# Performance work log

Measured on AMD Instinct MI355X. Metric: run time of the kernel, lower is better.

Reference implementation:

```python
import jax, jax.numpy as jnp
import numpy as np

B, D, H = 65536, 64, 512  # batch, input_dim (even), hidden_dim; num_layers=4 -> 4 Linears


def setup_inputs() -> dict:
    key = jax.random.key(0)
    ks = jax.random.split(key, 10)
    s_in = 1.0 / np.sqrt(D)
    s_h = 1.0 / np.sqrt(H)
    return {
        "t": jnp.zeros((1,), jnp.float32),
        "x": jax.random.normal(ks[0], (B, D), jnp.float32),
        "W0": jax.random.uniform(ks[1], (D, H), jnp.float32, -s_in, s_in),
        "b0": jax.random.uniform(ks[2], (H,), jnp.float32, -s_in, s_in),
        "W1": jax.random.uniform(ks[3], (H, H), jnp.float32, -s_h, s_h),
        "b1": jax.random.uniform(ks[4], (H,), jnp.float32, -s_h, s_h),
        "W2": jax.random.uniform(ks[5], (H, H), jnp.float32, -s_h, s_h),
        "b2": jax.random.uniform(ks[6], (H,), jnp.float32, -s_h, s_h),
        "W3": jax.random.uniform(ks[7], (H, 1), jnp.float32, -s_h, s_h),
        "b3": jax.random.uniform(ks[8], (1,), jnp.float32, -s_h, s_h),
    }


def reference(t, x, W0, b0, W1, b1, W2, b2, W3, b3):
    # Hamiltonian MLP: Linear->Tanh x3, final Linear to scalar energy per sample.
    def hamiltonian_sum(xx):
        h = jnp.tanh(xx @ W0 + b0)
        h = jnp.tanh(h @ W1 + b1)
        h = jnp.tanh(h @ W2 + b2)
        return jnp.sum(h @ W3 + b3)

    gradH = jax.grad(hamiltonian_sum)(x)  # [B, D]
    n = D // 2
    # gradH @ J.T with symplectic J == concat(gradH_p, -gradH_q)
    return jnp.concatenate([gradH[:, n:], -gradH[:, :n]], axis=1)
```

## Files before the change

### kernel.cpp

```cpp
#include <hip/hip_runtime.h>
#include <hip/hip_bf16.h>

typedef unsigned short u16;
typedef short s16x8 __attribute__((ext_vector_type(8)));
typedef float f32x4 __attribute__((ext_vector_type(4)));

#define MFMA_BF16(a, b, c) __builtin_amdgcn_mfma_f32_16x16x32_bf16((a), (b), (c), 0, 0, 0)

static constexpr int D_IN   = 64;
static constexpr int H_DIM  = 512;
static constexpr int M_TILE = 64;
static constexpr int AST    = 520;
static constexpr int XST    = 72;

__device__ __forceinline__ u16 f2bf(float f) {
  unsigned u = __builtin_bit_cast(unsigned, f);
  u += 0x7fffu + ((u >> 16) & 1u);
  return (u16)(u >> 16);
}
__device__ __forceinline__ float bfb2f(unsigned bits16) {
  return __builtin_bit_cast(float, bits16 << 16);
}
__device__ __forceinline__ float fast_tanh(float x) {
  float e = __expf(2.0f * x);
  return 1.0f - 2.0f * __builtin_amdgcn_rcpf(e + 1.0f);
}

__global__ __launch_bounds__(256) void prep_weights(const float* __restrict__ W0,
                                                    const float* __restrict__ W1,
                                                    const float* __restrict__ W2,
                                                    u16* __restrict__ ws) {
  u16* p0f = ws;
  u16* p0b = p0f + D_IN * H_DIM;
  u16* p1f = p0b + D_IN * H_DIM;
  u16* p1b = p1f + H_DIM * H_DIM;
  u16* p2f = p1b + H_DIM * H_DIM;
  u16* p2b = p2f + H_DIM * H_DIM;

  __shared__ __align__(16) u16 tile[64 * 72];

  int b = blockIdx.x;
  const float* src;
  u16 *dstf, *dstb;
  int rb, cb;
  bool isW0;
  if (b < 64) {
    src = W1; dstf = p1f; dstb = p1b; rb = b >> 3; cb = b & 7; isW0 = false;
  } else if (b < 128) {
    src = W2; dstf = p2f; dstb = p2b; rb = (b - 64) >> 3; cb = (b - 64) & 7; isW0 = false;
  } else {
    src = W0; dstf = p0f; dstb = p0b; rb = 0; cb = b - 128; isW0 = true;
  }

  const int tid = threadIdx.x;

  {
    int r = tid >> 2, cc = (tid & 3) * 16;
    const float4* s4 = (const float4*)(src + (size_t)(rb * 64 + r) * 512 + cb * 64 + cc);
    unsigned pk[8];
    #pragma unroll
    for (int v = 0; v < 4; ++v) {
      float4 f = s4[v];
      pk[v * 2]     = (unsigned)f2bf(f.x) | ((unsigned)f2bf(f.y) << 16);
      pk[v * 2 + 1] = (unsigned)f2bf(f.z) | ((unsigned)f2bf(f.w) << 16);
    }
    uint4* d = (uint4*)(tile + r * 72 + cc);
    d[0] = make_uint4(pk[0], pk[1], pk[2], pk[3]);
    d[1] = make_uint4(pk[4], pk[5], pk[6], pk[7]);
  }
  __syncthreads();

  const int c   = tid >> 6;
  const int kcl = (tid >> 5) & 1;
  const int ls  = (tid * 2) & 63;
  const int q   = ls >> 4;
  const int ln  = ls & 15;

  {
    __align__(16) u16 o[16];
    #pragma unroll
    for (int half = 0; half < 2; ++half)
      #pragma unroll
      for (int j = 0; j < 8; ++j)
        o[half * 8 + j] = tile[(kcl * 32 + q * 8 + j) * 72 + c * 16 + ln + half];
    int ntg   = 4 * cb + c;
    int kc    = 2 * rb + kcl;
    int chunk = isW0 ? (ntg * 2 + kc) : (ntg * 16 + kc);
    u16* dp = dstf + ((size_t)chunk * 64 + ls) * 8;
    *(uint4*)dp       = *(const uint4*)o;
    *(uint4*)(dp + 8) = *(const uint4*)(o + 8);
  }

  {
    const u16* rp = tile + (c * 16 + ln) * 72 + kcl * 32 + q * 8;
    s16x8 r0 = *(const s16x8*)rp;
    s16x8 r1 = *(const s16x8*)(rp + 72);
    int ntg = 4 * rb + c;
    int kc  = 2 * cb + kcl;
    u16* dp = dstb + ((size_t)(ntg * 16 + kc) * 64 + ls) * 8;
    *(s16x8*)dp       = r0;
    *(s16x8*)(dp + 8) = r1;
  }
}

#define LOAD_B4(BP, KC, BR)                                                     \
  {                                                                             \
    const u16* _sr = (BP) + ((size_t)wave << 15) + ((KC) << 9) + lane * 8;      \
    _Pragma("unroll")                                                           \
    for (int s = 0; s < 4; ++s)                                                 \
      (BR)[s] = *(const s16x8*)(_sr + (s << 13));                               \
  }

#define GEMM512_REG(BP)                                                         \
  {                                                                             \
    _Pragma("unroll") for (int mt = 0; mt < 4; ++mt)                            \
      _Pragma("unroll") for (int nt = 0; nt < 4; ++nt)                          \
        acc[mt][nt] = (f32x4){0.f, 0.f, 0.f, 0.f};                              \
    for (int kc2 = 0; kc2 < 8; ++kc2) {                                         \
      const int e = kc2 * 2;                                                    \
      {                                                                         \
        s16x8 a[4];                                                             \
        _Pragma("unroll")                                                       \
        for (int mt = 0; mt < 4; ++mt)                                          \
          a[mt] = *(const s16x8*)(buf + (mt * 16 + ln) * AST + e * 32 + q * 8); \
        _Pragma("unroll")                                                       \
        for (int nt = 0; nt < 4; ++nt)                                          \
          _Pragma("unroll")                                                     \
          for (int mt = 0; mt < 4; ++mt)                                        \
            acc[mt][nt] = MFMA_BF16(a[mt], bregA[nt], acc[mt][nt]);             \
        if (kc2 < 7) LOAD_B4(BP, e + 2, bregA);                                 \
      }                                                                         \
      const int o = e + 1;                                                      \
      {                                                                         \
        s16x8 a[4];                                                             \
        _Pragma("unroll")                                                       \
        for (int mt = 0; mt < 4; ++mt)                                          \
          a[mt] = *(const s16x8*)(buf + (mt * 16 + ln) * AST + o * 32 + q * 8); \
        _Pragma("unroll")                                                       \
        for (int nt = 0; nt < 4; ++nt)                                          \
          _Pragma("unroll")                                                     \
          for (int mt = 0; mt < 4; ++mt)                                        \
            acc[mt][nt] = MFMA_BF16(a[mt], bregB[nt], acc[mt][nt]);             \
        if (kc2 < 7) LOAD_B4(BP, o + 2, bregB);                                 \
      }                                                                         \
    }                                                                           \
  }

__global__ __launch_bounds__(512, 2) void hnn_fused(
    const float* __restrict__ x,
    const float* __restrict__ bias0,
    const float* __restrict__ bias1,
    const float* __restrict__ bias2,
    const float* __restrict__ W3,
    const u16* __restrict__ ws,
    float* __restrict__ out)
{
  const u16* p0f = ws;
  const u16* p0b = p0f + D_IN * H_DIM;
  const u16* p1f = p0b + D_IN * H_DIM;
  const u16* p1b = p1f + H_DIM * H_DIM;
  const u16* p2f = p1b + H_DIM * H_DIM;
  const u16* p2b = p2f + H_DIM * H_DIM;

  __shared__ __align__(16) u16 xs[M_TILE * XST];
  __shared__ __align__(16) u16 buf[M_TILE * AST];

  const int tid  = threadIdx.x;
  const int wave = tid >> 6;
  const int lane = tid & 63;
  const int ln   = lane & 15;
  const int q    = lane >> 4;
  const int nwb  = wave * 64;
  const int row0 = blockIdx.x * M_TILE;

  {
    int r = tid >> 3, c = (tid & 7) * 8;
    const float4* src = (const float4*)(x + (size_t)(row0 + r) * D_IN + c);
    float4 f0 = src[0];
    float4 f1 = src[1];
    u16* dst = xs + r * XST + c;
    dst[0] = f2bf(f0.x); dst[1] = f2bf(f0.y); dst[2] = f2bf(f0.z); dst[3] = f2bf(f0.w);
    dst[4] = f2bf(f1.x); dst[5] = f2bf(f1.y); dst[6] = f2bf(f1.z); dst[7] = f2bf(f1.w);
  }
  __syncthreads();

  f32x4 acc[4][4];
  s16x8 bregA[4], bregB[4];
  unsigned h0p[4][4][2];
  unsigned h1p[4][4][2];
  float bias[4];

  #pragma unroll
  for (int nt = 0; nt < 4; ++nt) bias[nt] = bias0[nwb + nt * 16 + ln];
  #pragma unroll
  for (int mt = 0; mt < 4; ++mt)
    #pragma unroll
    for (int nt = 0; nt < 4; ++nt) acc[mt][nt] = (f32x4){0.f, 0.f, 0.f, 0.f};
  {
    const u16* bpw0 = p0f + (wave << 12) + lane * 8;
    #pragma unroll
    for (int kc = 0; kc < 2; ++kc) {
      s16x8 a[4];
      #pragma unroll
      for (int mt = 0; mt < 4; ++mt)
        a[mt] = *(const s16x8*)(xs + (mt * 16 + ln) * XST + kc * 32 + q * 8);
      #pragma unroll
      for (int nt = 0; nt < 4; ++nt) {
        s16x8 b = *(const s16x8*)(bpw0 + (nt << 10) + (kc << 9));
        #pragma unroll
        for (int mt = 0; mt < 4; ++mt)
          acc[mt][nt] = MFMA_BF16(a[mt], b, acc[mt][nt]);
      }
    }
  }
  LOAD_B4(p1f, 0, bregA);
  LOAD_B4(p1f, 1, bregB);
  #pragma unroll
  for (int mt = 0; mt < 4; ++mt)
    #pragma unroll
    for (int nt = 0; nt < 4; ++nt) {
      int col = nwb + nt * 16 + ln;
      u16 u[4];
      #pragma unroll
      for (int r = 0; r < 4; ++r) {
        float th = fast_tanh(acc[mt][nt][r] + bias[nt]);
        u[r] = f2bf(th);
        buf[(mt * 16 + q * 4 + r) * AST + col] = u[r];
      }
      h0p[mt][nt][0] = (unsigned)u[0] | ((unsigned)u[1] << 16);
      h0p[mt][nt][1] = (unsigned)u[2] | ((unsigned)u[3] << 16);
    }
  __syncthreads();

  #pragma unroll
  for (int nt = 0; nt < 4; ++nt) bias[nt] = bias1[nwb + nt * 16 + ln];
  GEMM512_REG(p1f);
  __syncthreads();
  LOAD_B4(p2f, 0, bregA);
  LOAD_B4(p2f, 1, bregB);
  #pragma unroll
  for (int mt = 0; mt < 4; ++mt)
    #pragma unroll
    for (int nt = 0; nt < 4; ++nt) {
      int col = nwb + nt * 16 + ln;
      u16 u[4];
      #pragma unroll
      for (int r = 0; r < 4; ++r) {
        float th = fast_tanh(acc[mt][nt][r] + bias[nt]);
        u[r] = f2bf(th);
        buf[(mt * 16 + q * 4 + r) * AST + col] = u[r];
      }
      h1p[mt][nt][0] = (unsigned)u[0] | ((unsigned)u[1] << 16);
      h1p[mt][nt][1] = (unsigned)u[2] | ((unsigned)u[3] << 16);
    }
  __syncthreads();

  #pragma unroll
  for (int nt = 0; nt < 4; ++nt) bias[nt] = bias2[nwb + nt * 16 + ln];
  float w3v[4];
  #pragma unroll
  for (int nt = 0; nt < 4; ++nt) w3v[nt] = W3[nwb + nt * 16 + ln];
  GEMM512_REG(p2f);
  __syncthreads();
  LOAD_B4(p2b, 0, bregA);
  LOAD_B4(p2b, 1, bregB);
  #pragma unroll
  for (int mt = 0; mt < 4; ++mt)
    #pragma unroll
    for (int nt = 0; nt < 4; ++nt) {
      int col = nwb + nt * 16 + ln;
      #pragma unroll
      for (int r = 0; r < 4; ++r) {
        float th = fast_tanh(acc[mt][nt][r] + bias[nt]);
        float gz = w3v[nt] * (1.0f - th * th);
        buf[(mt * 16 + q * 4 + r) * AST + col] = f2bf(gz);
      }
    }
  __syncthreads();

  GEMM512_REG(p2b);
  __syncthreads();
  LOAD_B4(p1b, 0, bregA);
  LOAD_B4(p1b, 1, bregB);
  #pragma unroll
  for (int mt = 0; mt < 4; ++mt)
    #pragma unroll
    for (int nt = 0; nt < 4; ++nt) {
      int col = nwb + nt * 16 + ln;
      unsigned pa = h1p[mt][nt][0], pb = h1p[mt][nt][1];
      float hh[4] = { bfb2f(pa & 0xffffu), bfb2f(pa >> 16),
                      bfb2f(pb & 0xffffu), bfb2f(pb >> 16) };
      #pragma unroll
      for (int r = 0; r < 4; ++r) {
        float gz = acc[mt][nt][r] * (1.0f - hh[r] * hh[r]);
        buf[(mt * 16 + q * 4 + r) * AST + col] = f2bf(gz);
      }
    }
  __syncthreads();

  GEMM512_REG(p1b);
  __syncthreads();
  #pragma unroll
  for (int mt = 0; mt < 4; ++mt)
    #pragma unroll
    for (int nt = 0; nt < 4; ++nt) {
      int col = nwb + nt * 16 + ln;
      unsigned pa = h0p[mt][nt][0], pb = h0p[mt][nt][1];
      float hh[4] = { bfb2f(pa & 0xffffu), bfb2f(pa >> 16),
                      bfb2f(pb & 0xffffu), bfb2f(pb >> 16) };
      #pragma unroll
      for (int r = 0; r < 4; ++r) {
        float gz = acc[mt][nt][r] * (1.0f - hh[r] * hh[r]);
        buf[(mt * 16 + q * 4 + r) * AST + col] = f2bf(gz);
      }
    }
  __syncthreads();

  {
    f32x4 acc5[2];
    acc5[0] = (f32x4){0.f, 0.f, 0.f, 0.f};
    acc5[1] = (f32x4){0.f, 0.f, 0.f, 0.f};
    const int mt5 = wave & 3;
    const int nb5 = (wave >> 2) * 32;
    const u16* bp5 = p0b + ((wave >> 2) << 14) + lane * 8;
    #pragma unroll 2
    for (int kc = 0; kc < 16; ++kc) {
      s16x8 a = *(const s16x8*)(buf + (mt5 * 16 + ln) * AST + kc * 32 + q * 8);
      #pragma unroll
      for (int nt = 0; nt < 2; ++nt) {
        s16x8 b = *(const s16x8*)(bp5 + (nt << 13) + (kc << 9));
        acc5[nt] = MFMA_BF16(a, b, acc5[nt]);
      }
    }
    #pragma unroll
    for (int nt = 0; nt < 2; ++nt) {
      int g = nb5 + nt * 16 + ln;
      int c = (g < 32) ? g + 32 : g - 32;
      float s = (g < 32) ? -1.0f : 1.0f;
      #pragma unroll
      for (int r = 0; r < 4; ++r) {
        int grow = row0 + mt5 * 16 + q * 4 + r;
        out[(size_t)grow * 64 + c] = s * acc5[nt][r];
      }
    }
  }
}

extern "C" void kernel_launch(void* const* d_in, const int* in_sizes, int n_in,
                              void* d_out, int out_size, void* d_ws, size_t ws_size,
                              hipStream_t stream) {
  const float* x  = (const float*)d_in[1];
  const float* W0 = (const float*)d_in[2];
  const float* b0 = (const float*)d_in[3];
  const float* W1 = (const float*)d_in[4];
  const float* b1 = (const float*)d_in[5];
  const float* W2 = (const float*)d_in[6];
  const float* b2 = (const float*)d_in[7];
  const float* W3 = (const float*)d_in[8];
  u16* ws = (u16*)d_ws;
  float* out = (float*)d_out;

  prep_weights<<<136, 256, 0, stream>>>(W0, W1, W2, ws);
  hnn_fused<<<65536 / M_TILE, 512, 0, stream>>>(x, b0, b1, b2, W3, ws, out);
}
```

Baseline: 228.1 us.

## Switch hidden-layer GEMMs to 32x32x16 bf16 MFMA with matching weight layout

Replaces the 16x16x32 MFMA tiling (4x4 tiles per wave) with 32x32x16 MFMA (2x2 tiles per wave) for the forward and backward 512-wide GEMMs and the first layer. The weight prep kernel is changed to emit packed weights in the 32-wide N / 16-deep K chunk layout the larger MFMA expects, while W0's backward copy keeps the old layout. The larger instruction halves the number of A and B fragment loads from LDS and global memory per output and the count of issued MFMAs, at the cost of more complex epilogue indexing. The x staging store is also packed into one 16-byte LDS write.

```diff
diff --git a/kernel.cpp b/kernel.cpp
--- a/kernel.cpp
+++ b/kernel.cpp
@@ -4,8 +4,10 @@
 typedef unsigned short u16;
 typedef short s16x8 __attribute__((ext_vector_type(8)));
 typedef float f32x4 __attribute__((ext_vector_type(4)));
+typedef float f32x16 __attribute__((ext_vector_type(16)));
 
 #define MFMA_BF16(a, b, c) __builtin_amdgcn_mfma_f32_16x16x32_bf16((a), (b), (c), 0, 0, 0)
+#define MFMA32(a, b, c)    __builtin_amdgcn_mfma_f32_32x32x16_bf16((a), (b), (c), 0, 0, 0)
 
 static constexpr int D_IN   = 64;
 static constexpr int H_DIM  = 512;
@@ -24,6 +26,10 @@
 __device__ __forceinline__ float fast_tanh(float x) {
   float e = __expf(2.0f * x);
   return 1.0f - 2.0f * __builtin_amdgcn_rcpf(e + 1.0f);
+}
+__device__ __forceinline__ f32x16 zero16() {
+  f32x16 z = {0.f,0.f,0.f,0.f,0.f,0.f,0.f,0.f,0.f,0.f,0.f,0.f,0.f,0.f,0.f,0.f};
+  return z;
 }
 
 __global__ __launch_bounds__(256) void prep_weights(const float* __restrict__ W0,
@@ -70,78 +76,89 @@
   }
   __syncthreads();
 
-  const int c   = tid >> 6;
-  const int kcl = (tid >> 5) & 1;
-  const int ls  = (tid * 2) & 63;
-  const int q   = ls >> 4;
-  const int ln  = ls & 15;
+  const int cl    = tid >> 5;
+  const int nt32l = cl >> 2;
+  const int k16l  = cl & 3;
+  const int ls    = (tid & 31) * 2;
+  const int q5    = ls >> 5;
+  const int l31   = ls & 31;
 
   {
     __align__(16) u16 o[16];
     #pragma unroll
-    for (int half = 0; half < 2; ++half)
+    for (int p = 0; p < 2; ++p)
       #pragma unroll
       for (int j = 0; j < 8; ++j)
-        o[half * 8 + j] = tile[(kcl * 32 + q * 8 + j) * 72 + c * 16 + ln + half];
-    int ntg   = 4 * cb + c;
-    int kc    = 2 * rb + kcl;
-    int chunk = isW0 ? (ntg * 2 + kc) : (ntg * 16 + kc);
+        o[p * 8 + j] = tile[(k16l * 16 + q5 * 8 + j) * 72 + nt32l * 32 + l31 + p];
+    int K16MAX = isW0 ? 4 : 32;
+    int chunk = (2 * cb + nt32l) * K16MAX + (4 * rb + k16l);
     u16* dp = dstf + ((size_t)chunk * 64 + ls) * 8;
     *(uint4*)dp       = *(const uint4*)o;
     *(uint4*)(dp + 8) = *(const uint4*)(o + 8);
   }
 
-  {
+  if (!isW0) {
+    const u16* rp = tile + (nt32l * 32 + l31) * 72 + k16l * 16 + q5 * 8;
+    s16x8 r0 = *(const s16x8*)rp;
+    s16x8 r1 = *(const s16x8*)(rp + 72);
+    int chunk = (2 * rb + nt32l) * 32 + (4 * cb + k16l);
+    u16* dp = dstb + ((size_t)chunk * 64 + ls) * 8;
+    *(s16x8*)dp       = r0;
+    *(s16x8*)(dp + 8) = r1;
+  } else {
+    const int c   = tid >> 6;
+    const int kcl = (tid >> 5) & 1;
+    const int ls2 = (tid * 2) & 63;
+    const int q   = ls2 >> 4;
+    const int ln  = ls2 & 15;
     const u16* rp = tile + (c * 16 + ln) * 72 + kcl * 32 + q * 8;
     s16x8 r0 = *(const s16x8*)rp;
     s16x8 r1 = *(const s16x8*)(rp + 72);
-    int ntg = 4 * rb + c;
-    int kc  = 2 * cb + kcl;
-    u16* dp = dstb + ((size_t)(ntg * 16 + kc) * 64 + ls) * 8;
+    int kc = 2 * cb + kcl;
+    u16* dp = dstb + ((size_t)(c * 16 + kc) * 64 + ls2) * 8;
     *(s16x8*)dp       = r0;
     *(s16x8*)(dp + 8) = r1;
   }
 }
 
-#define LOAD_B4(BP, KC, BR)                                                     \
+#define LOAD_B2(BP, KS, BR)                                                     \
   {                                                                             \
-    const u16* _sr = (BP) + ((size_t)wave << 15) + ((KC) << 9) + lane * 8;      \
-    _Pragma("unroll")                                                           \
-    for (int s = 0; s < 4; ++s)                                                 \
-      (BR)[s] = *(const s16x8*)(_sr + (s << 13));                               \
-  }
-
-#define GEMM512_REG(BP)                                                         \
+    const u16* _sr = (BP) + ((size_t)wave << 15) + ((KS) << 9) + lane * 8;      \
+    (BR)[0] = *(const s16x8*)(_sr);                                             \
+    (BR)[1] = *(const s16x8*)(_sr + (1 << 14));                                 \
+  }
+
+#define GEMM512_32(BP)                                                          \
   {                                                                             \
-    _Pragma("unroll") for (int mt = 0; mt < 4; ++mt)                            \
-      _Pragma("unroll") for (int nt = 0; nt < 4; ++nt)                          \
-        acc[mt][nt] = (f32x4){0.f, 0.f, 0.f, 0.f};                              \
-    for (int kc2 = 0; kc2 < 8; ++kc2) {                                         \
-      const int e = kc2 * 2;                                                    \
+    _Pragma("unroll") for (int mt = 0; mt < 2; ++mt)                            \
+      _Pragma("unroll") for (int nt = 0; nt < 2; ++nt)                          \
+        acc[mt][nt] = zero16();                                                 \
+    for (int ks2 = 0; ks2 < 16; ++ks2) {                                        \
+      const int e = ks2 * 2;                                                    \
       {                                                                         \
-        s16x8 a[4];                                                             \
+        s16x8 a[2];                                                             \
         _Pragma("unroll")                                                       \
-        for (int mt = 0; mt < 4; ++mt)                                          \
-          a[mt] = *(const s16x8*)(buf + (mt * 16 + ln) * AST + e * 32 + q * 8); \
+        for (int mt = 0; mt < 2; ++mt)                                          \
+          a[mt] = *(const s16x8*)(buf + (mt * 32 + l31) * AST + e * 16 + q5 * 8); \
         _Pragma("unroll")                                                       \
-        for (int nt = 0; nt < 4; ++nt)                                          \
+        for (int nt = 0; nt < 2; ++nt)                                          \
           _Pragma("unroll")                                                     \
-          for (int mt = 0; mt < 4; ++mt)                                        \
-            acc[mt][nt] = MFMA_BF16(a[mt], bregA[nt], acc[mt][nt]);             \
-        if (kc2 < 7) LOAD_B4(BP, e + 2, bregA);                                 \
+          for (int mt = 0; mt < 2; ++mt)                                        \
+            acc[mt][nt] = MFMA32(a[mt], bregA[nt], acc[mt][nt]);                \
+        if (ks2 < 15) LOAD_B2(BP, e + 2, bregA);                                \
       }                                                                         \
       const int o = e + 1;                                                      \
       {                                                                         \
-        s16x8 a[4];                                                             \
+        s16x8 a[2];                                                             \
         _Pragma("unroll")                                                       \
-        for (int mt = 0; mt < 4; ++mt)                                          \
-          a[mt] = *(const s16x8*)(buf + (mt * 16 + ln) * AST + o * 32 + q * 8); \
+        for (int mt = 0; mt < 2; ++mt)                                          \
+          a[mt] = *(const s16x8*)(buf + (mt * 32 + l31) * AST + o * 16 + q5 * 8); \
         _Pragma("unroll")                                                       \
-        for (int nt = 0; nt < 4; ++nt)                                          \
+        for (int nt = 0; nt < 2; ++nt)                                          \
           _Pragma("unroll")                                                     \
-          for (int mt = 0; mt < 4; ++mt)                                        \
-            acc[mt][nt] = MFMA_BF16(a[mt], bregB[nt], acc[mt][nt]);             \
-        if (kc2 < 7) LOAD_B4(BP, o + 2, bregB);                                 \
+          for (int mt = 0; mt < 2; ++mt)                                        \
+            acc[mt][nt] = MFMA32(a[mt], bregB[nt], acc[mt][nt]);                \
+        if (ks2 < 15) LOAD_B2(BP, o + 2, bregB);                                \
       }                                                                         \
     }                                                                           \
   }
@@ -170,6 +187,8 @@
   const int lane = tid & 63;
   const int ln   = lane & 15;
   const int q    = lane >> 4;
+  const int l31  = lane & 31;
+  const int q5   = lane >> 5;
   const int nwb  = wave * 64;
   const int row0 = blockIdx.x * M_TILE;
 
@@ -178,141 +197,167 @@
     const float4* src = (const float4*)(x + (size_t)(row0 + r) * D_IN + c);
     float4 f0 = src[0];
     float4 f1 = src[1];
-    u16* dst = xs + r * XST + c;
-    dst[0] = f2bf(f0.x); dst[1] = f2bf(f0.y); dst[2] = f2bf(f0.z); dst[3] = f2bf(f0.w);
-    dst[4] = f2bf(f1.x); dst[5] = f2bf(f1.y); dst[6] = f2bf(f1.z); dst[7] = f2bf(f1.w);
-  }
-  __syncthreads();
-
-  f32x4 acc[4][4];
-  s16x8 bregA[4], bregB[4];
-  unsigned h0p[4][4][2];
-  unsigned h1p[4][4][2];
-  float bias[4];
+    unsigned pk0 = (unsigned)f2bf(f0.x) | ((unsigned)f2bf(f0.y) << 16);
+    unsigned pk1 = (unsigned)f2bf(f0.z) | ((unsigned)f2bf(f0.w) << 16);
+    unsigned pk2 = (unsigned)f2bf(f1.x) | ((unsigned)f2bf(f1.y) << 16);
+    unsigned pk3 = (unsigned)f2bf(f1.z) | ((unsigned)f2bf(f1.w) << 16);
+    uint4* dst = (uint4*)(xs + r * XST + c);
+    *dst = make_uint4(pk0, pk1, pk2, pk3);
+  }
+  __syncthreads();
+
+  f32x16 acc[2][2];
+  s16x8 bregA[2], bregB[2];
+  unsigned h0p[2][2][8];
+  unsigned h1p[2][2][8];
 
   #pragma unroll
-  for (int nt = 0; nt < 4; ++nt) bias[nt] = bias0[nwb + nt * 16 + ln];
+  for (int mt = 0; mt < 2; ++mt)
+    #pragma unroll
+    for (int nt = 0; nt < 2; ++nt) acc[mt][nt] = zero16();
+  {
+    const u16* bpw0 = p0f + ((size_t)wave << 12) + lane * 8;
+    #pragma unroll
+    for (int ks = 0; ks < 4; ++ks) {
+      s16x8 a[2];
+      #pragma unroll
+      for (int mt = 0; mt < 2; ++mt)
+        a[mt] = *(const s16x8*)(xs + (mt * 32 + l31) * XST + ks * 16 + q5 * 8);
+      #pragma unroll
+      for (int nt = 0; nt < 2; ++nt) {
+        s16x8 b = *(const s16x8*)(bpw0 + (nt << 11) + (ks << 9));
+        #pragma unroll
+        for (int mt = 0; mt < 2; ++mt)
+          acc[mt][nt] = MFMA32(a[mt], b, acc[mt][nt]);
+      }
+    }
+  }
+  LOAD_B2(p1f, 0, bregA);
+  LOAD_B2(p1f, 1, bregB);
+  {
+    float bv[2];
+    #pragma unroll
+    for (int nt = 0; nt < 2; ++nt) bv[nt] = bias0[nwb + nt * 32 + l31];
+    #pragma unroll
+    for (int mt = 0; mt < 2; ++mt)
+      #pragma unroll
+      for (int nt = 0; nt < 2; ++nt) {
+        int col = nwb + nt * 32 + l31;
+        u16* bp = buf + (mt * 32 + q5 * 4) * AST + col;
+        #pragma unroll
+        for (int g = 0; g < 4; ++g) {
+          u16 u[4];
+          #pragma unroll
+          for (int r = 0; r < 4; ++r) {
+            float th = fast_tanh(acc[mt][nt][g * 4 + r] + bv[nt]);
+            u[r] = f2bf(th);
+            bp[(g * 8 + r) * AST] = u[r];
+          }
+          h0p[mt][nt][g * 2]     = (unsigned)u[0] | ((unsigned)u[1] << 16);
+          h0p[mt][nt][g * 2 + 1] = (unsigned)u[2] | ((unsigned)u[3] << 16);
+        }
+      }
+  }
+  __syncthreads();
+
+  GEMM512_32(p1f);
+  __syncthreads();
+  LOAD_B2(p2f, 0, bregA);
+  LOAD_B2(p2f, 1, bregB);
+  {
+    float bv[2];
+    #pragma unroll
+    for (int nt = 0; nt < 2; ++nt) bv[nt] = bias1[nwb + nt * 32 + l31];
+    #pragma unroll
+    for (int mt = 0; mt < 2; ++mt)
+      #pragma unroll
+      for (int nt = 0; nt < 2; ++nt) {
+        int col = nwb + nt * 32 + l31;
+        u16* bp = buf + (mt * 32 + q5 * 4) * AST + col;
+        #pragma unroll
+        for (int g = 0; g < 4; ++g) {
+          u16 u[4];
+          #pragma unroll
+          for (int r = 0; r < 4; ++r) {
+            float th = fast_tanh(acc[mt][nt][g * 4 + r] + bv[nt]);
+            u[r] = f2bf(th);
+            bp[(g * 8 + r) * AST] = u[r];
+          }
+          h1p[mt][nt][g * 2]     = (unsigned)u[0] | ((unsigned)u[1] << 16);
+          h1p[mt][nt][g * 2 + 1] = (unsigned)u[2] | ((unsigned)u[3] << 16);
+        }
+      }
+  }
+  __syncthreads();
+
+  GEMM512_32(p2f);
+  __syncthreads();
+  LOAD_B2(p2b, 0, bregA);
+  LOAD_B2(p2b, 1, bregB);
+  {
+    float bv[2], w3v[2];
+    #pragma unroll
+    for (int nt = 0; nt < 2; ++nt) {
+      bv[nt]  = bias2[nwb + nt * 32 + l31];
+      w3v[nt] = W3[nwb + nt * 32 + l31];
+    }
+    #pragma unroll
+    for (int mt = 0; mt < 2; ++mt)
+      #pragma unroll
+      for (int nt = 0; nt < 2; ++nt) {
+        int col = nwb + nt * 32 + l31;
+        u16* bp = buf + (mt * 32 + q5 * 4) * AST + col;
+        #pragma unroll
+        for (int g = 0; g < 4; ++g)
+          #pragma unroll
+          for (int r = 0; r < 4; ++r) {
+            float th = fast_tanh(acc[mt][nt][g * 4 + r] + bv[nt]);
+            float gz = w3v[nt] * (1.0f - th * th);
+            bp[(g * 8 + r) * AST] = f2bf(gz);
+          }
+      }
+  }
+  __syncthreads();
+
+  GEMM512_32(p2b);
+  __syncthreads();
+  LOAD_B2(p1b, 0, bregA);
+  LOAD_B2(p1b, 1, bregB);
   #pragma unroll
-  for (int mt = 0; mt < 4; ++mt)
-    #pragma unroll
-    for (int nt = 0; nt < 4; ++nt) acc[mt][nt] = (f32x4){0.f, 0.f, 0.f, 0.f};
-  {
-    const u16* bpw0 = p0f + (wave << 12) + lane * 8;
-    #pragma unroll
-    for (int kc = 0; kc < 2; ++kc) {
-      s16x8 a[4];
-      #pragma unroll
-      for (int mt = 0; mt < 4; ++mt)
-        a[mt] = *(const s16x8*)(xs + (mt * 16 + ln) * XST + kc * 32 + q * 8);
-      #pragma unroll
-      for (int nt = 0; nt < 4; ++nt) {
-        s16x8 b = *(const s16x8*)(bpw0 + (nt << 10) + (kc << 9));
-        #pragma unroll
-        for (int mt = 0; mt < 4; ++mt)
-          acc[mt][nt] = MFMA_BF16(a[mt], b, acc[mt][nt]);
-      }
-    }
-  }
-  LOAD_B4(p1f, 0, bregA);
-  LOAD_B4(p1f, 1, bregB);
+  for (int mt = 0; mt < 2; ++mt)
+    #pragma unroll
+    for (int nt = 0; nt < 2; ++nt) {
+      int col = nwb + nt * 32 + l31;
+      u16* bp = buf + (mt * 32 + q5 * 4) * AST + col;
+      #pragma unroll
+      for (int g = 0; g < 4; ++g)
+        #pragma unroll
+        for (int r = 0; r < 4; ++r) {
+          unsigned pk = h1p[mt][nt][g * 2 + (r >> 1)];
+          float hh = bfb2f((r & 1) ? (pk >> 16) : (pk & 0xffffu));
+          float gz = acc[mt][nt][g * 4 + r] * (1.0f - hh * hh);
+          bp[(g * 8 + r) * AST] = f2bf(gz);
+        }
+    }
+  __syncthreads();
+
+  GEMM512_32(p1b);
+  __syncthreads();
   #pragma unroll
-  for (int mt = 0; mt < 4; ++mt)
-    #pragma unroll
-    for (int nt = 0; nt < 4; ++nt) {
-      int col = nwb + nt * 16 + ln;
-      u16 u[4];
-      #pragma unroll
-      for (int r = 0; r < 4; ++r) {
-        float th = fast_tanh(acc[mt][nt][r] + bias[nt]);
-        u[r] = f2bf(th);
-        buf[(mt * 16 + q * 4 + r) * AST + col] = u[r];
-      }
-      h0p[mt][nt][0] = (unsigned)u[0] | ((unsigned)u[1] << 16);
-      h0p[mt][nt][1] = (unsigned)u[2] | ((unsigned)u[3] << 16);
-    }
-  __syncthreads();
-
-  #pragma unroll
-  for (int nt = 0; nt < 4; ++nt) bias[nt] = bias1[nwb + nt * 16 + ln];
-  GEMM512_REG(p1f);
-  __syncthreads();
-  LOAD_B4(p2f, 0, bregA);
-  LOAD_B4(p2f, 1, bregB);
-  #pragma unroll
-  for (int mt = 0; mt < 4; ++mt)
-    #pragma unroll
-    for (int nt = 0; nt < 4; ++nt) {
-      int col = nwb + nt * 16 + ln;
-      u16 u[4];
-      #pragma unroll
-      for (int r = 0; r < 4; ++r) {
-        float th = fast_tanh(acc[mt][nt][r] + bias[nt]);
-        u[r] = f2bf(th);
-        buf[(mt * 16 + q * 4 + r) * AST + col] = u[r];
-      }
-      h1p[mt][nt][0] = (unsigned)u[0] | ((unsigned)u[1] << 16);
-      h1p[mt][nt][1] = (unsigned)u[2] | ((unsigned)u[3] << 16);
-    }
-  __syncthreads();
-
-  #pragma unroll
-  for (int nt = 0; nt < 4; ++nt) bias[nt] = bias2[nwb + nt * 16 + ln];
-  float w3v[4];
-  #pragma unroll
-  for (int nt = 0; nt < 4; ++nt) w3v[nt] = W3[nwb + nt * 16 + ln];
-  GEMM512_REG(p2f);
-  __syncthreads();
-  LOAD_B4(p2b, 0, bregA);
-  LOAD_B4(p2b, 1, bregB);
-  #pragma unroll
-  for (int mt = 0; mt < 4; ++mt)
-    #pragma unroll
-    for (int nt = 0; nt < 4; ++nt) {
-      int col = nwb + nt * 16 + ln;
-      #pragma unroll
-      for (int r = 0; r < 4; ++r) {
-        float th = fast_tanh(acc[mt][nt][r] + bias[nt]);
-        float gz = w3v[nt] * (1.0f - th * th);
-        buf[(mt * 16 + q * 4 + r) * AST + col] = f2bf(gz);
-      }
-    }
-  __syncthreads();
-
-  GEMM512_REG(p2b);
-  __syncthreads();
-  LOAD_B4(p1b, 0, bregA);
-  LOAD_B4(p1b, 1, bregB);
-  #pragma unroll
-  for (int mt = 0; mt < 4; ++mt)
-    #pragma unroll
-    for (int nt = 0; nt < 4; ++nt) {
-      int col = nwb + nt * 16 + ln;
-      unsigned pa = h1p[mt][nt][0], pb = h1p[mt][nt][1];
-      float hh[4] = { bfb2f(pa & 0xffffu), bfb2f(pa >> 16),
-                      bfb2f(pb & 0xffffu), bfb2f(pb >> 16) };
-      #pragma unroll
-      for (int r = 0; r < 4; ++r) {
-        float gz = acc[mt][nt][r] * (1.0f - hh[r] * hh[r]);
-        buf[(mt * 16 + q * 4 + r) * AST + col] = f2bf(gz);
-      }
-    }
-  __syncthreads();
-
-  GEMM512_REG(p1b);
-  __syncthreads();
-  #pragma unroll
-  for (int mt = 0; mt < 4; ++mt)
-    #pragma unroll
-    for (int nt = 0; nt < 4; ++nt) {
-      int col = nwb + nt * 16 + ln;
-      unsigned pa = h0p[mt][nt][0], pb = h0p[mt][nt][1];
-      float hh[4] = { bfb2f(pa & 0xffffu), bfb2f(pa >> 16),
-                      bfb2f(pb & 0xffffu), bfb2f(pb >> 16) };
-      #pragma unroll
-      for (int r = 0; r < 4; ++r) {
-        float gz = acc[mt][nt][r] * (1.0f - hh[r] * hh[r]);
-        buf[(mt * 16 + q * 4 + r) * AST + col] = f2bf(gz);
-      }
+  for (int mt = 0; mt < 2; ++mt)
+    #pragma unroll
+    for (int nt = 0; nt < 2; ++nt) {
+      int col = nwb + nt * 32 + l31;
+      u16* bp = buf + (mt * 32 + q5 * 4) * AST + col;
+      #pragma unroll
+      for (int g = 0; g < 4; ++g)
+        #pragma unroll
+        for (int r = 0; r < 4; ++r) {
+          unsigned pk = h0p[mt][nt][g * 2 + (r >> 1)];
+          float hh = bfb2f((r & 1) ? (pk >> 16) : (pk & 0xffffu));
+          float gz = acc[mt][nt][g * 4 + r] * (1.0f - hh * hh);
+          bp[(g * 8 + r) * AST] = f2bf(gz);
+        }
     }
   __syncthreads();
 
```

Result: slower. 260.0 us (+14.0%).

## Split row tile into two halves and overlap each epilogue with the other half's GEMM

Applied to the files above, without the earlier changes.

The 64-row block tile is split into two 32-row sub-tiles with separate accumulators and ping-pong LDS buffers. Each sub-tile's tanh or derivative epilogue is interleaved into the K-loop of the other sub-tile's GEMM, so VALU and LDS-store work overlaps MFMA instead of running in its own barrier-separated phase. Biases and W3 are loaded once up front. The cost is that each B-register load now serves only 32 rows, so weight traffic from L2 doubles, LDS use grows, and the extra accumulators and packed activations add register pressure that could cause spills.

```diff
diff --git a/kernel.cpp b/kernel.cpp
--- a/kernel.cpp
+++ b/kernel.cpp
@@ -111,39 +111,82 @@
       (BR)[s] = *(const s16x8*)(_sr + (s << 13));                               \
   }
 
-#define GEMM512_REG(BP)                                                         \
-  {                                                                             \
-    _Pragma("unroll") for (int mt = 0; mt < 4; ++mt)                            \
-      _Pragma("unroll") for (int nt = 0; nt < 4; ++nt)                          \
-        acc[mt][nt] = (f32x4){0.f, 0.f, 0.f, 0.f};                              \
-    for (int kc2 = 0; kc2 < 8; ++kc2) {                                         \
-      const int e = kc2 * 2;                                                    \
-      {                                                                         \
-        s16x8 a[4];                                                             \
-        _Pragma("unroll")                                                       \
-        for (int mt = 0; mt < 4; ++mt)                                          \
-          a[mt] = *(const s16x8*)(buf + (mt * 16 + ln) * AST + e * 32 + q * 8); \
-        _Pragma("unroll")                                                       \
-        for (int nt = 0; nt < 4; ++nt)                                          \
-          _Pragma("unroll")                                                     \
-          for (int mt = 0; mt < 4; ++mt)                                        \
-            acc[mt][nt] = MFMA_BF16(a[mt], bregA[nt], acc[mt][nt]);             \
-        if (kc2 < 7) LOAD_B4(BP, e + 2, bregA);                                 \
-      }                                                                         \
-      const int o = e + 1;                                                      \
-      {                                                                         \
-        s16x8 a[4];                                                             \
-        _Pragma("unroll")                                                       \
-        for (int mt = 0; mt < 4; ++mt)                                          \
-          a[mt] = *(const s16x8*)(buf + (mt * 16 + ln) * AST + o * 32 + q * 8); \
-        _Pragma("unroll")                                                       \
-        for (int nt = 0; nt < 4; ++nt)                                          \
-          _Pragma("unroll")                                                     \
-          for (int mt = 0; mt < 4; ++mt)                                        \
-            acc[mt][nt] = MFMA_BF16(a[mt], bregB[nt], acc[mt][nt]);             \
-        if (kc2 < 7) LOAD_B4(BP, o + 2, bregB);                                 \
-      }                                                                         \
-    }                                                                           \
+#define ZACC(ACC)                                                               \
+  _Pragma("unroll") for (int zm = 0; zm < 2; ++zm)                              \
+    _Pragma("unroll") for (int zn = 0; zn < 4; ++zn)                            \
+      ACC[zm][zn] = (f32x4){0.f, 0.f, 0.f, 0.f};
+
+#define EPI_H(MT, NT, ACC, HP, BV, DB)                                          \
+  {                                                                             \
+    float t0_ = fast_tanh(ACC[MT][NT][0] + BV[NT]);                             \
+    float t1_ = fast_tanh(ACC[MT][NT][1] + BV[NT]);                             \
+    float t2_ = fast_tanh(ACC[MT][NT][2] + BV[NT]);                             \
+    float t3_ = fast_tanh(ACC[MT][NT][3] + BV[NT]);                             \
+    u16 u0_ = f2bf(t0_), u1_ = f2bf(t1_), u2_ = f2bf(t2_), u3_ = f2bf(t3_);     \
+    u16* bp_ = (DB) + ((MT) * 16 + q * 4) * AST + nwb + (NT) * 16 + ln;         \
+    bp_[0] = u0_; bp_[AST] = u1_; bp_[2 * AST] = u2_; bp_[3 * AST] = u3_;       \
+    HP[MT][NT][0] = (unsigned)u0_ | ((unsigned)u1_ << 16);                      \
+    HP[MT][NT][1] = (unsigned)u2_ | ((unsigned)u3_ << 16);                      \
+  }
+#define EPI_G2(MT, NT, ACC, DB)                                                 \
+  {                                                                             \
+    u16* bp_ = (DB) + ((MT) * 16 + q * 4) * AST + nwb + (NT) * 16 + ln;         \
+    float t0_ = fast_tanh(ACC[MT][NT][0] + b2v[NT]);                            \
+    float t1_ = fast_tanh(ACC[MT][NT][1] + b2v[NT]);                            \
+    float t2_ = fast_tanh(ACC[MT][NT][2] + b2v[NT]);                            \
+    float t3_ = fast_tanh(ACC[MT][NT][3] + b2v[NT]);                            \
+    bp_[0]       = f2bf(w3v[NT] * (1.0f - t0_ * t0_));                          \
+    bp_[AST]     = f2bf(w3v[NT] * (1.0f - t1_ * t1_));                          \
+    bp_[2 * AST] = f2bf(w3v[NT] * (1.0f - t2_ * t2_));                          \
+    bp_[3 * AST] = f2bf(w3v[NT] * (1.0f - t3_ * t3_));                          \
+  }
+#define EPI_B(MT, NT, ACC, HP, DB)                                              \
+  {                                                                             \
+    unsigned pa_ = HP[MT][NT][0], pb_ = HP[MT][NT][1];                          \
+    float h0_ = bfb2f(pa_ & 0xffffu), h1_ = bfb2f(pa_ >> 16);                   \
+    float h2_ = bfb2f(pb_ & 0xffffu), h3_ = bfb2f(pb_ >> 16);                   \
+    u16* bp_ = (DB) + ((MT) * 16 + q * 4) * AST + nwb + (NT) * 16 + ln;         \
+    bp_[0]       = f2bf(ACC[MT][NT][0] * (1.0f - h0_ * h0_));                   \
+    bp_[AST]     = f2bf(ACC[MT][NT][1] * (1.0f - h1_ * h1_));                   \
+    bp_[2 * AST] = f2bf(ACC[MT][NT][2] * (1.0f - h2_ * h2_));                   \
+    bp_[3 * AST] = f2bf(ACC[MT][NT][3] * (1.0f - h3_ * h3_));                   \
+  }
+#define EPI_NONE(MT, NT) {}
+
+#define KSTEP(RB, ACC, BP, K2, EPIU)                                            \
+  {                                                                             \
+    s16x8 a0_ = *(const s16x8*)((RB) + (ln) * AST + (K2) * 64 + q * 8);         \
+    s16x8 a1_ = *(const s16x8*)((RB) + (16 + ln) * AST + (K2) * 64 + q * 8);    \
+    ACC[0][0] = MFMA_BF16(a0_, bregA[0], ACC[0][0]);                            \
+    ACC[1][0] = MFMA_BF16(a1_, bregA[0], ACC[1][0]);                            \
+    ACC[0][1] = MFMA_BF16(a0_, bregA[1], ACC[0][1]);                            \
+    ACC[1][1] = MFMA_BF16(a1_, bregA[1], ACC[1][1]);                            \
+    ACC[0][2] = MFMA_BF16(a0_, bregA[2], ACC[0][2]);                            \
+    ACC[1][2] = MFMA_BF16(a1_, bregA[2], ACC[1][2]);                            \
+    ACC[0][3] = MFMA_BF16(a0_, bregA[3], ACC[0][3]);                            \
+    ACC[1][3] = MFMA_BF16(a1_, bregA[3], ACC[1][3]);                            \
+    if ((K2) < 7) LOAD_B4(BP, (K2) * 2 + 2, bregA);                             \
+    EPIU((K2) >> 2, (K2) & 3);                                                  \
+    s16x8 a2_ = *(const s16x8*)((RB) + (ln) * AST + (K2) * 64 + 32 + q * 8);    \
+    s16x8 a3_ = *(const s16x8*)((RB) + (16 + ln) * AST + (K2) * 64 + 32 + q * 8); \
+    ACC[0][0] = MFMA_BF16(a2_, bregB[0], ACC[0][0]);                            \
+    ACC[1][0] = MFMA_BF16(a3_, bregB[0], ACC[1][0]);                            \
+    ACC[0][1] = MFMA_BF16(a2_, bregB[1], ACC[0][1]);                            \
+    ACC[1][1] = MFMA_BF16(a3_, bregB[1], ACC[1][1]);                            \
+    ACC[0][2] = MFMA_BF16(a2_, bregB[2], ACC[0][2]);                            \
+    ACC[1][2] = MFMA_BF16(a3_, bregB[2], ACC[1][2]);                            \
+    ACC[0][3] = MFMA_BF16(a2_, bregB[3], ACC[0][3]);                            \
+    ACC[1][3] = MFMA_BF16(a3_, bregB[3], ACC[1][3]);                            \
+    if ((K2) < 7) LOAD_B4(BP, (K2) * 2 + 3, bregB);                             \
+  }
+
+#define GEMMF(RB, ACC, BP, EPIU)                                                \
+  {                                                                             \
+    ZACC(ACC);                                                                  \
+    KSTEP(RB, ACC, BP, 0, EPIU); KSTEP(RB, ACC, BP, 1, EPIU);                   \
+    KSTEP(RB, ACC, BP, 2, EPIU); KSTEP(RB, ACC, BP, 3, EPIU);                   \
+    KSTEP(RB, ACC, BP, 4, EPIU); KSTEP(RB, ACC, BP, 5, EPIU);                   \
+    KSTEP(RB, ACC, BP, 6, EPIU); KSTEP(RB, ACC, BP, 7, EPIU);                   \
   }
 
 __global__ __launch_bounds__(512, 2) void hnn_fused(
@@ -163,7 +206,10 @@
   const u16* p2b = p2f + H_DIM * H_DIM;
 
   __shared__ __align__(16) u16 xs[M_TILE * XST];
-  __shared__ __align__(16) u16 buf[M_TILE * AST];
+  __shared__ __align__(16) u16 bufA0[32 * AST];
+  __shared__ __align__(16) u16 bufB0[32 * AST];
+  __shared__ __align__(16) u16 bufA1[32 * AST];
+  __shared__ __align__(16) u16 bufB1[32 * AST];
 
   const int tid  = threadIdx.x;
   const int wave = tid >> 6;
@@ -182,166 +228,148 @@
     dst[0] = f2bf(f0.x); dst[1] = f2bf(f0.y); dst[2] = f2bf(f0.z); dst[3] = f2bf(f0.w);
     dst[4] = f2bf(f1.x); dst[5] = f2bf(f1.y); dst[6] = f2bf(f1.z); dst[7] = f2bf(f1.w);
   }
-  __syncthreads();
-
-  f32x4 acc[4][4];
+
+  float b0v[4], b1v[4], b2v[4], w3v[4];
+  #pragma unroll
+  for (int nt = 0; nt < 4; ++nt) {
+    b0v[nt] = bias0[nwb + nt * 16 + ln];
+    b1v[nt] = bias1[nwb + nt * 16 + ln];
+    b2v[nt] = bias2[nwb + nt * 16 + ln];
+    w3v[nt] = W3[nwb + nt * 16 + ln];
+  }
+  __syncthreads();
+
+  f32x4 accA[2][4], accB[2][4];
   s16x8 bregA[4], bregB[4];
-  unsigned h0p[4][4][2];
-  unsigned h1p[4][4][2];
-  float bias[4];
-
-  #pragma unroll
-  for (int nt = 0; nt < 4; ++nt) bias[nt] = bias0[nwb + nt * 16 + ln];
-  #pragma unroll
-  for (int mt = 0; mt < 4; ++mt)
-    #pragma unroll
-    for (int nt = 0; nt < 4; ++nt) acc[mt][nt] = (f32x4){0.f, 0.f, 0.f, 0.f};
+  unsigned h0pA[2][4][2], h0pB[2][4][2];
+  unsigned h1pA[2][4][2], h1pB[2][4][2];
+
+  ZACC(accA);
   {
     const u16* bpw0 = p0f + (wave << 12) + lane * 8;
     #pragma unroll
     for (int kc = 0; kc < 2; ++kc) {
-      s16x8 a[4];
-      #pragma unroll
-      for (int mt = 0; mt < 4; ++mt)
-        a[mt] = *(const s16x8*)(xs + (mt * 16 + ln) * XST + kc * 32 + q * 8);
+      s16x8 a0 = *(const s16x8*)(xs + (ln) * XST + kc * 32 + q * 8);
+      s16x8 a1 = *(const s16x8*)(xs + (16 + ln) * XST + kc * 32 + q * 8);
       #pragma unroll
       for (int nt = 0; nt < 4; ++nt) {
         s16x8 b = *(const s16x8*)(bpw0 + (nt << 10) + (kc << 9));
-        #pragma unroll
-        for (int mt = 0; mt < 4; ++mt)
-          acc[mt][nt] = MFMA_BF16(a[mt], b, acc[mt][nt]);
+        accA[0][nt] = MFMA_BF16(a0, b, accA[0][nt]);
+        accA[1][nt] = MFMA_BF16(a1, b, accA[1][nt]);
       }
     }
   }
   LOAD_B4(p1f, 0, bregA);
   LOAD_B4(p1f, 1, bregB);
-  #pragma unroll
-  for (int mt = 0; mt < 4; ++mt)
-    #pragma unroll
-    for (int nt = 0; nt < 4; ++nt) {
-      int col = nwb + nt * 16 + ln;
-      u16 u[4];
+
+  ZACC(accB);
+  {
+    const u16* bpw0 = p0f + (wave << 12) + lane * 8;
+    #pragma unroll
+    for (int kc = 0; kc < 2; ++kc) {
+      s16x8 a0 = *(const s16x8*)(xs + (32 + ln) * XST + kc * 32 + q * 8);
+      s16x8 a1 = *(const s16x8*)(xs + (48 + ln) * XST + kc * 32 + q * 8);
       #pragma unroll
-      for (int r = 0; r < 4; ++r) {
-        float th = fast_tanh(acc[mt][nt][r] + bias[nt]);
-        u[r] = f2bf(th);
-        buf[(mt * 16 + q * 4 + r) * AST + col] = u[r];
+      for (int nt = 0; nt < 4; ++nt) {
+        s16x8 b = *(const s16x8*)(bpw0 + (nt << 10) + (kc << 9));
+        accB[0][nt] = MFMA_BF16(a0, b, accB[0][nt]);
+        accB[1][nt] = MFMA_BF16(a1, b, accB[1][nt]);
       }
-      h0p[mt][nt][0] = (unsigned)u[0] | ((unsigned)u[1] << 16);
-      h0p[mt][nt][1] = (unsigned)u[2] | ((unsigned)u[3] << 16);
-    }
-  __syncthreads();
-
-  #pragma unroll
-  for (int nt = 0; nt < 4; ++nt) bias[nt] = bias1[nwb + nt * 16 + ln];
-  GEMM512_REG(p1f);
-  __syncthreads();
+    }
+  }
+  EPI_H(0, 0, accA, h0pA, b0v, bufA0); EPI_H(0, 1, accA, h0pA, b0v, bufA0);
+  EPI_H(0, 2, accA, h0pA, b0v, bufA0); EPI_H(0, 3, accA, h0pA, b0v, bufA0);
+  EPI_H(1, 0, accA, h0pA, b0v, bufA0); EPI_H(1, 1, accA, h0pA, b0v, bufA0);
+  EPI_H(1, 2, accA, h0pA, b0v, bufA0); EPI_H(1, 3, accA, h0pA, b0v, bufA0);
+  __syncthreads();
+
+  #define EPI0T1(MT, NT) EPI_H(MT, NT, accB, h0pB, b0v, bufA1)
+  GEMMF(bufA0, accA, p1f, EPI0T1);
+  LOAD_B4(p1f, 0, bregA);
+  LOAD_B4(p1f, 1, bregB);
+  __syncthreads();
+
+  #define EPI1T0(MT, NT) EPI_H(MT, NT, accA, h1pA, b1v, bufB0)
+  GEMMF(bufA1, accB, p1f, EPI1T0);
   LOAD_B4(p2f, 0, bregA);
   LOAD_B4(p2f, 1, bregB);
-  #pragma unroll
-  for (int mt = 0; mt < 4; ++mt)
-    #pragma unroll
-    for (int nt = 0; nt < 4; ++nt) {
-      int col = nwb + nt * 16 + ln;
-      u16 u[4];
-      #pragma unroll
-      for (int r = 0; r < 4; ++r) {
-        float th = fast_tanh(acc[mt][nt][r] + bias[nt]);
-        u[r] = f2bf(th);
-        buf[(mt * 16 + q * 4 + r) * AST + col] = u[r];
-      }
-      h1p[mt][nt][0] = (unsigned)u[0] | ((unsigned)u[1] << 16);
-      h1p[mt][nt][1] = (unsigned)u[2] | ((unsigned)u[3] << 16);
-    }
-  __syncthreads();
-
-  #pragma unroll
-  for (int nt = 0; nt < 4; ++nt) bias[nt] = bias2[nwb + nt * 16 + ln];
-  float w3v[4];
-  #pragma unroll
-  for (int nt = 0; nt < 4; ++nt) w3v[nt] = W3[nwb + nt * 16 + ln];
-  GEMM512_REG(p2f);
-  __syncthreads();
+  __syncthreads();
+
+  #define EPI1T1(MT, NT) EPI_H(MT, NT, accB, h1pB, b1v, bufB1)
+  GEMMF(bufB0, accA, p2f, EPI1T1);
+  LOAD_B4(p2f, 0, bregA);
+  LOAD_B4(p2f, 1, bregB);
+  __syncthreads();
+
+  #define EPI2T0(MT, NT) EPI_G2(MT, NT, accA, bufA0)
+  GEMMF(bufB1, accB, p2f, EPI2T0);
   LOAD_B4(p2b, 0, bregA);
   LOAD_B4(p2b, 1, bregB);
-  #pragma unroll
-  for (int mt = 0; mt < 4; ++mt)
-    #pragma unroll
-    for (int nt = 0; nt < 4; ++nt) {
-      int col = nwb + nt * 16 + ln;
-      #pragma unroll
-      for (int r = 0; r < 4; ++r) {
-        float th = fast_tanh(acc[mt][nt][r] + bias[nt]);
-        float gz = w3v[nt] * (1.0f - th * th);
-        buf[(mt * 16 + q * 4 + r) * AST + col] = f2bf(gz);
-      }
-    }
-  __syncthreads();
-
-  GEMM512_REG(p2b);
-  __syncthreads();
+  __syncthreads();
+
+  #define EPI2T1(MT, NT) EPI_G2(MT, NT, accB, bufA1)
+  GEMMF(bufA0, accA, p2b, EPI2T1);
+  LOAD_B4(p2b, 0, bregA);
+  LOAD_B4(p2b, 1, bregB);
+  __syncthreads();
+
+  #define EPI3T0(MT, NT) EPI_B(MT, NT, accA, h1pA, bufB0)
+  GEMMF(bufA1, accB, p2b, EPI3T0);
   LOAD_B4(p1b, 0, bregA);
   LOAD_B4(p1b, 1, bregB);
-  #pragma unroll
-  for (int mt = 0; mt < 4; ++mt)
-    #pragma unroll
-    for (int nt = 0; nt < 4; ++nt) {
-      int col = nwb + nt * 16 + ln;
-      unsigned pa = h1p[mt][nt][0], pb = h1p[mt][nt][1];
-      float hh[4] = { bfb2f(pa & 0xffffu), bfb2f(pa >> 16),
-                      bfb2f(pb & 0xffffu), bfb2f(pb >> 16) };
-      #pragma unroll
-      for (int r = 0; r < 4; ++r) {
-        float gz = acc[mt][nt][r] * (1.0f - hh[r] * hh[r]);
-        buf[(mt * 16 + q * 4 + r) * AST + col] = f2bf(gz);
-      }
-    }
-  __syncthreads();
-
-  GEMM512_REG(p1b);
-  __syncthreads();
-  #pragma unroll
-  for (int mt = 0; mt < 4; ++mt)
-    #pragma unroll
-    for (int nt = 0; nt < 4; ++nt) {
-      int col = nwb + nt * 16 + ln;
-      unsigned pa = h0p[mt][nt][0], pb = h0p[mt][nt][1];
-      float hh[4] = { bfb2f(pa & 0xffffu), bfb2f(pa >> 16),
-                      bfb2f(pb & 0xffffu), bfb2f(pb >> 16) };
-      #pragma unroll
-      for (int r = 0; r < 4; ++r) {
-        float gz = acc[mt][nt][r] * (1.0f - hh[r] * hh[r]);
-        buf[(mt * 16 + q * 4 + r) * AST + col] = f2bf(gz);
-      }
-    }
-  __syncthreads();
-
-  {
-    f32x4 acc5[2];
-    acc5[0] = (f32x4){0.f, 0.f, 0.f, 0.f};
-    acc5[1] = (f32x4){0.f, 0.f, 0.f, 0.f};
-    const int mt5 = wave & 3;
-    const int nb5 = (wave >> 2) * 32;
-    const u16* bp5 = p0b + ((wave >> 2) << 14) + lane * 8;
-    #pragma unroll 2
+  __syncthreads();
+
+  #define EPI3T1(MT, NT) EPI_B(MT, NT, accB, h1pB, bufB1)
+  GEMMF(bufB0, accA, p1b, EPI3T1);
+  LOAD_B4(p1b, 0, bregA);
+  LOAD_B4(p1b, 1, bregB);
+  __syncthreads();
+
+  #define EPI4T0(MT, NT) EPI_B(MT, NT, accA, h0pA, bufA0)
+  GEMMF(bufB1, accB, p1b, EPI4T0);
+  __syncthreads();
+
+  const int mt5 = wave & 1;
+  const int c5  = wave >> 1;
+  const u16* bp5 = p0b + ((size_t)c5 << 13) + lane * 8;
+  {
+    f32x4 acc5 = (f32x4){0.f, 0.f, 0.f, 0.f};
+    #pragma unroll
     for (int kc = 0; kc < 16; ++kc) {
-      s16x8 a = *(const s16x8*)(buf + (mt5 * 16 + ln) * AST + kc * 32 + q * 8);
-      #pragma unroll
-      for (int nt = 0; nt < 2; ++nt) {
-        s16x8 b = *(const s16x8*)(bp5 + (nt << 13) + (kc << 9));
-        acc5[nt] = MFMA_BF16(a, b, acc5[nt]);
-      }
-    }
-    #pragma unroll
-    for (int nt = 0; nt < 2; ++nt) {
-      int g = nb5 + nt * 16 + ln;
-      int c = (g < 32) ? g + 32 : g - 32;
-      float s = (g < 32) ? -1.0f : 1.0f;
-      #pragma unroll
-      for (int r = 0; r < 4; ++r) {
-        int grow = row0 + mt5 * 16 + q * 4 + r;
-        out[(size_t)grow * 64 + c] = s * acc5[nt][r];
-      }
+      s16x8 a = *(const s16x8*)(bufA0 + (mt5 * 16 + ln) * AST + kc * 32 + q * 8);
+      s16x8 b = *(const s16x8*)(bp5 + (kc << 9));
+      acc5 = MFMA_BF16(a, b, acc5);
+    }
+    EPI_B(0, 0, accB, h0pB, bufA1); EPI_B(0, 1, accB, h0pB, bufA1);
+    EPI_B(0, 2, accB, h0pB, bufA1); EPI_B(0, 3, accB, h0pB, bufA1);
+    EPI_B(1, 0, accB, h0pB, bufA1); EPI_B(1, 1, accB, h0pB, bufA1);
+    EPI_B(1, 2, accB, h0pB, bufA1); EPI_B(1, 3, accB, h0pB, bufA1);
+    int g = c5 * 16 + ln;
+    int cc = (g < 32) ? g + 32 : g - 32;
+    float sg = (g < 32) ? -1.0f : 1.0f;
+    #pragma unroll
+    for (int r = 0; r < 4; ++r) {
+      int grow = row0 + mt5 * 16 + q * 4 + r;
+      out[(size_t)grow * 64 + cc] = sg * acc5[r];
+    }
+  }
+  __syncthreads();
+
+  {
+    f32x4 acc5 = (f32x4){0.f, 0.f, 0.f, 0.f};
+    #pragma unroll
+    for (int kc = 0; kc < 16; ++kc) {
+      s16x8 a = *(const s16x8*)(bufA1 + (mt5 * 16 + ln) * AST + kc * 32 + q * 8);
+      s16x8 b = *(const s16x8*)(bp5 + (kc << 9));
+      acc5 = MFMA_BF16(a, b, acc5);
+    }
+    int g = c5 * 16 + ln;
+    int cc = (g < 32) ? g + 32 : g - 32;
+    float sg = (g < 32) ? -1.0f : 1.0f;
+    #pragma unroll
+    for (int r = 0; r < 4; ++r) {
+      int grow = row0 + 32 + mt5 * 16 + q * 4 + r;
+      out[(size_t)grow * 64 + cc] = sg * acc5[r];
     }
   }
 }
```

After: 332.6 us. +45.8%, slower.
